# Optimization experiments

Measured on AMD Instinct MI355X. Metric: run time of the kernel, lower is better.

## Reference

```python
import itertools
import jax, jax.numpy as jnp
import numpy as np

GRID = 16384      # self.shape = (GRID,)
LAYERS = 8        # num_layers
SPAN = 2          # span = (2,)
K = 2 * SPAN + 1  # kernel size = 5 (ninputs)
NPOS = 2 ** K     # 32 possible boolean input combos
BATCH = 32
M = 4096          # x width; GRID % M == 0
STRIDE = GRID // M

# bitmask: all 2^K boolean input combinations, shape (NPOS, K)
_BITMASK = jnp.asarray(list(itertools.product(range(2), repeat=K)), dtype=jnp.float32)


def setup_inputs() -> dict:
    key = jax.random.key(0)
    k1, k2 = jax.random.split(key)
    x = jax.random.uniform(k1, (BATCH, M), dtype=jnp.float32)
    toggle_gates = jax.random.uniform(k2, (LAYERS, NPOS, GRID), dtype=jnp.float32)
    return {"x": x, "toggle_gates": toggle_gates}


def _convolve(state):
    # torch convolve(): offsets 0..K-1 via wrap-around roll, then spatial roll by
    # -SPAN to center the window -> neighbor n+i-SPAN (mod GRID) at kernel idx i.
    # jnp.roll(state, SPAN - i) gives out[:, n] = state[:, n + i - SPAN mod GRID].
    return jnp.stack([jnp.roll(state, SPAN - i, axis=1) for i in range(K)], axis=-1)  # (B, N, K)


def reference(x, toggle_gates):
    tw = jax.nn.sigmoid(toggle_gates)  # (L, NPOS, N)
    # embed(): scatter x evenly into the grid, rest is scratch (zeros)
    state = jnp.zeros((x.shape[0], GRID), dtype=x.dtype).at[:, ::STRIDE].set(x)

    def step(s, tw_layer):
        conv = _convolve(s)  # (B, N, K)
        # weight[c, b, n] = prod_i (1 - |bitmask[c, i] - conv[b, n, i]|)
        w = jnp.prod(1.0 - jnp.abs(_BITMASK[:, None, None, :] - conv[None]), axis=-1)  # (C, B, N)
        new = jnp.clip(jnp.einsum('cbn,cn->bn', w, tw_layer), 0.0, 1.0)
        return new, None

    state, _ = jax.lax.scan(step, state, tw)
    # forward returns state[slices] = state[:, ::STRIDE]
    return state[:, ::STRIDE]
```

## Files before the change

kernel.cpp:

```cpp
#include <hip/hip_runtime.h>

#define GRID_N 16384
#define NLAYERS 8
#define NPOS 32
#define BATCH 32
#define MW 4096
#define TILE 32
#define HALO 16
#define WBUF 64
#define ROWP 36

typedef float f2 __attribute__((ext_vector_type(2)));

__device__ __forceinline__ float dpp_shr1(float v) {
    return __builtin_bit_cast(float, __builtin_amdgcn_update_dpp(
        0, __builtin_bit_cast(int, v), 0x138, 0xF, 0xF, true));
}
__device__ __forceinline__ float dpp_shl1(float v) {
    return __builtin_bit_cast(float, __builtin_amdgcn_update_dpp(
        0, __builtin_bit_cast(int, v), 0x130, 0xF, 0xF, true));
}
__device__ __forceinline__ f2 shr1(f2 v) { f2 r; r.x = dpp_shr1(v.x); r.y = dpp_shr1(v.y); return r; }
__device__ __forceinline__ f2 shl1(f2 v) { f2 r; r.x = dpp_shl1(v.x); r.y = dpp_shl1(v.y); return r; }

__device__ __forceinline__ float sigm(float v) {
    return __builtin_amdgcn_rcpf(1.0f + __expf(-v));
}

__device__ __forceinline__ void barrier_lds_only() {
    asm volatile("s_waitcnt lgkmcnt(0)\n\ts_barrier" ::: "memory");
}

__global__ __launch_bounds__(512, 4) void ASIC_44186623541335_kernel(
    const float* __restrict__ x,
    const float* __restrict__ tg,
    float* __restrict__ out)
{
    __shared__ __align__(16) float twl[4][WBUF][ROWP];

    const int tid = threadIdx.x;
    const int tx  = tid & 63;
    const int w   = tid >> 6;
    const int c0  = 4 * w;
    const int start = blockIdx.x * TILE;
    const int gcol  = (start - HALO + tx) & (GRID_N - 1);

    const bool on = (gcol & 3) == 0;
    const int  m  = gcol >> 2;
    float xv[4];
    #pragma unroll
    for (int k = 0; k < 4; ++k)
        xv[k] = on ? x[(c0 + k) * MW + m] : 0.0f;

    float pf[32];
    #pragma unroll
    for (int l = 0; l < NLAYERS; ++l)
        #pragma unroll
        for (int k = 0; k < 4; ++k)
            pf[l * 4 + k] = tg[((size_t)l * NPOS + c0 + k) * GRID_N + gcol];

    f2 S[2];
    S[0].x = xv[0]; S[0].y = xv[1];
    S[1].x = xv[2]; S[1].y = xv[3];

    #pragma unroll
    for (int l4 = 0; l4 < 4; ++l4) {
        float4 sg;
        sg.x = sigm(pf[l4 * 4 + 0]);
        sg.y = sigm(pf[l4 * 4 + 1]);
        sg.z = sigm(pf[l4 * 4 + 2]);
        sg.w = sigm(pf[l4 * 4 + 3]);
        *(float4*)&twl[l4][tx][c0] = sg;
    }
    barrier_lds_only();

    for (int l = 0; l < NLAYERS; ++l) {
        f2 s0v[2], s1v[2], s3v[2], s4v[2];
        #pragma unroll
        for (int q = 0; q < 2; ++q) {
            s1v[q] = shr1(S[q]);
            s0v[q] = shr1(s1v[q]);
            s3v[q] = shl1(S[q]);
            s4v[q] = shl1(s3v[q]);
        }

        f2 u0[16], u1[16];
        #pragma unroll
        for (int k = 0; k < 8; ++k) {
            const float4 t4 = *(const float4*)&twl[l & 3][tx][4 * k];
            const float dA = t4.y - t4.x;
            const float dB = t4.w - t4.z;
            u0[2 * k]     = __builtin_elementwise_fma(s4v[0], (f2)dA, (f2)t4.x);
            u0[2 * k + 1] = __builtin_elementwise_fma(s4v[0], (f2)dB, (f2)t4.z);
            u1[2 * k]     = __builtin_elementwise_fma(s4v[1], (f2)dA, (f2)t4.x);
            u1[2 * k + 1] = __builtin_elementwise_fma(s4v[1], (f2)dB, (f2)t4.z);
        }

        #pragma unroll
        for (int q = 0; q < 2; ++q) {
            f2* u = q ? u1 : u0;
            #pragma unroll
            for (int r = 0; r < 8; ++r)
                u[r] = __builtin_elementwise_fma(s3v[q], u[2 * r + 1] - u[2 * r], u[2 * r]);
            #pragma unroll
            for (int r = 0; r < 4; ++r)
                u[r] = __builtin_elementwise_fma(S[q],   u[2 * r + 1] - u[2 * r], u[2 * r]);
            #pragma unroll
            for (int r = 0; r < 2; ++r)
                u[r] = __builtin_elementwise_fma(s1v[q], u[2 * r + 1] - u[2 * r], u[2 * r]);
            f2 rv = __builtin_elementwise_fma(s0v[q], u[1] - u[0], u[0]);
            rv = __builtin_elementwise_min(__builtin_elementwise_max(rv, (f2)0.0f), (f2)1.0f);
            S[q] = rv;
        }

        if (l == 3) {
            barrier_lds_only();
            #pragma unroll
            for (int l4 = 0; l4 < 4; ++l4) {
                float4 sg;
                sg.x = sigm(pf[16 + l4 * 4 + 0]);
                sg.y = sigm(pf[16 + l4 * 4 + 1]);
                sg.z = sigm(pf[16 + l4 * 4 + 2]);
                sg.w = sigm(pf[16 + l4 * 4 + 3]);
                *(float4*)&twl[l4][tx][c0] = sg;
            }
            barrier_lds_only();
        }
    }

    const int rel = tx - HALO;
    if (rel >= 0 && rel < TILE && (rel & 3) == 0) {
        const int mo = (start >> 2) + (rel >> 2);
        out[(c0 + 0) * MW + mo] = S[0].x;
        out[(c0 + 1) * MW + mo] = S[0].y;
        out[(c0 + 2) * MW + mo] = S[1].x;
        out[(c0 + 3) * MW + mo] = S[1].y;
    }
}

extern "C" void kernel_launch(void* const* d_in, const int* in_sizes, int n_in,
                              void* d_out, int out_size, void* d_ws, size_t ws_size,
                              hipStream_t stream) {
    const float* x  = (const float*)d_in[0];
    const float* tg = (const float*)d_in[1];
    float* out = (float*)d_out;
    ASIC_44186623541335_kernel<<<GRID_N / TILE, 512, 0, stream>>>(x, tg, out);
}
```

Baseline: 80.29 us.

## Stream toggle-gate weights in two-layer groups with rolling register prefetch

```diff
diff --git a/kernel.cpp b/kernel.cpp
--- a/kernel.cpp
+++ b/kernel.cpp
@@ -36,7 +36,7 @@
     const float* __restrict__ tg,
     float* __restrict__ out)
 {
-    __shared__ __align__(16) float twl[4][WBUF][ROWP];
+    __shared__ __align__(16) float twl[2][WBUF][ROWP];
 
     const int tid = threadIdx.x;
     const int tx  = tid & 63;
@@ -52,77 +52,99 @@
     for (int k = 0; k < 4; ++k)
         xv[k] = on ? x[(c0 + k) * MW + m] : 0.0f;
 
-    float pf[32];
+    float pfA[8], pfB[8];
     #pragma unroll
-    for (int l = 0; l < NLAYERS; ++l)
+    for (int ll = 0; ll < 2; ++ll)
         #pragma unroll
         for (int k = 0; k < 4; ++k)
-            pf[l * 4 + k] = tg[((size_t)l * NPOS + c0 + k) * GRID_N + gcol];
+            pfA[ll * 4 + k] = tg[((size_t)ll * NPOS + c0 + k) * GRID_N + gcol];
+    #pragma unroll
+    for (int ll = 0; ll < 2; ++ll)
+        #pragma unroll
+        for (int k = 0; k < 4; ++k)
+            pfB[ll * 4 + k] = tg[((size_t)(2 + ll) * NPOS + c0 + k) * GRID_N + gcol];
 
     f2 S[2];
     S[0].x = xv[0]; S[0].y = xv[1];
     S[1].x = xv[2]; S[1].y = xv[3];
 
     #pragma unroll
-    for (int l4 = 0; l4 < 4; ++l4) {
+    for (int ll = 0; ll < 2; ++ll) {
         float4 sg;
-        sg.x = sigm(pf[l4 * 4 + 0]);
-        sg.y = sigm(pf[l4 * 4 + 1]);
-        sg.z = sigm(pf[l4 * 4 + 2]);
-        sg.w = sigm(pf[l4 * 4 + 3]);
-        *(float4*)&twl[l4][tx][c0] = sg;
+        sg.x = sigm(pfA[ll * 4 + 0]);
+        sg.y = sigm(pfA[ll * 4 + 1]);
+        sg.z = sigm(pfA[ll * 4 + 2]);
+        sg.w = sigm(pfA[ll * 4 + 3]);
+        *(float4*)&twl[ll][tx][c0] = sg;
     }
+    #pragma unroll
+    for (int ll = 0; ll < 2; ++ll)
+        #pragma unroll
+        for (int k = 0; k < 4; ++k)
+            pfA[ll * 4 + k] = tg[((size_t)(4 + ll) * NPOS + c0 + k) * GRID_N + gcol];
     barrier_lds_only();
 
-    for (int l = 0; l < NLAYERS; ++l) {
-        f2 s0v[2], s1v[2], s3v[2], s4v[2];
+    #pragma unroll
+    for (int g = 0; g < 4; ++g) {
         #pragma unroll
-        for (int q = 0; q < 2; ++q) {
-            s1v[q] = shr1(S[q]);
-            s0v[q] = shr1(s1v[q]);
-            s3v[q] = shl1(S[q]);
-            s4v[q] = shl1(s3v[q]);
+        for (int ll = 0; ll < 2; ++ll) {
+            f2 s0v[2], s1v[2], s3v[2], s4v[2];
+            #pragma unroll
+            for (int q = 0; q < 2; ++q) {
+                s1v[q] = shr1(S[q]);
+                s0v[q] = shr1(s1v[q]);
+                s3v[q] = shl1(S[q]);
+                s4v[q] = shl1(s3v[q]);
+            }
+
+            f2 u0[16], u1[16];
+            #pragma unroll
+            for (int k = 0; k < 8; ++k) {
+                const float4 t4 = *(const float4*)&twl[ll][tx][4 * k];
+                const float dA = t4.y - t4.x;
+                const float dB = t4.w - t4.z;
+                u0[2 * k]     = __builtin_elementwise_fma(s4v[0], (f2)dA, (f2)t4.x);
+                u0[2 * k + 1] = __builtin_elementwise_fma(s4v[0], (f2)dB, (f2)t4.z);
+                u1[2 * k]     = __builtin_elementwise_fma(s4v[1], (f2)dA, (f2)t4.x);
+                u1[2 * k + 1] = __builtin_elementwise_fma(s4v[1], (f2)dB, (f2)t4.z);
+            }
+
+            #pragma unroll
+            for (int q = 0; q < 2; ++q) {
+                f2* u = q ? u1 : u0;
+                #pragma unroll
+                for (int r = 0; r < 8; ++r)
+                    u[r] = __builtin_elementwise_fma(s3v[q], u[2 * r + 1] - u[2 * r], u[2 * r]);
+                #pragma unroll
+                for (int r = 0; r < 4; ++r)
+                    u[r] = __builtin_elementwise_fma(S[q],   u[2 * r + 1] - u[2 * r], u[2 * r]);
+                #pragma unroll
+                for (int r = 0; r < 2; ++r)
+                    u[r] = __builtin_elementwise_fma(s1v[q], u[2 * r + 1] - u[2 * r], u[2 * r]);
+                f2 rv = __builtin_elementwise_fma(s0v[q], u[1] - u[0], u[0]);
+                rv = __builtin_elementwise_min(__builtin_elementwise_max(rv, (f2)0.0f), (f2)1.0f);
+                S[q] = rv;
+            }
         }
 
-        f2 u0[16], u1[16];
-        #pragma unroll
-        for (int k = 0; k < 8; ++k) {
-            const float4 t4 = *(const float4*)&twl[l & 3][tx][4 * k];
-            const float dA = t4.y - t4.x;
-            const float dB = t4.w - t4.z;
-            u0[2 * k]     = __builtin_elementwise_fma(s4v[0], (f2)dA, (f2)t4.x);
-            u0[2 * k + 1] = __builtin_elementwise_fma(s4v[0], (f2)dB, (f2)t4.z);
-            u1[2 * k]     = __builtin_elementwise_fma(s4v[1], (f2)dA, (f2)t4.x);
-            u1[2 * k + 1] = __builtin_elementwise_fma(s4v[1], (f2)dB, (f2)t4.z);
-        }
-
-        #pragma unroll
-        for (int q = 0; q < 2; ++q) {
-            f2* u = q ? u1 : u0;
+        if (g < 3) {
+            barrier_lds_only();
+            float* pfs = (g & 1) ? pfA : pfB;
             #pragma unroll
-            for (int r = 0; r < 8; ++r)
-                u[r] = __builtin_elementwise_fma(s3v[q], u[2 * r + 1] - u[2 * r], u[2 * r]);
-            #pragma unroll
-            for (int r = 0; r < 4; ++r)
-                u[r] = __builtin_elementwise_fma(S[q],   u[2 * r + 1] - u[2 * r], u[2 * r]);
-            #pragma unroll
-            for (int r = 0; r < 2; ++r)
-                u[r] = __builtin_elementwise_fma(s1v[q], u[2 * r + 1] - u[2 * r], u[2 * r]);
-            f2 rv = __builtin_elementwise_fma(s0v[q], u[1] - u[0], u[0]);
-            rv = __builtin_elementwise_min(__builtin_elementwise_max(rv, (f2)0.0f), (f2)1.0f);
-            S[q] = rv;
-        }
-
-        if (l == 3) {
-            barrier_lds_only();
-            #pragma unroll
-            for (int l4 = 0; l4 < 4; ++l4) {
+            for (int ll = 0; ll < 2; ++ll) {
                 float4 sg;
-                sg.x = sigm(pf[16 + l4 * 4 + 0]);
-                sg.y = sigm(pf[16 + l4 * 4 + 1]);
-                sg.z = sigm(pf[16 + l4 * 4 + 2]);
-                sg.w = sigm(pf[16 + l4 * 4 + 3]);
-                *(float4*)&twl[l4][tx][c0] = sg;
+                sg.x = sigm(pfs[ll * 4 + 0]);
+                sg.y = sigm(pfs[ll * 4 + 1]);
+                sg.z = sigm(pfs[ll * 4 + 2]);
+                sg.w = sigm(pfs[ll * 4 + 3]);
+                *(float4*)&twl[ll][tx][c0] = sg;
+            }
+            if (g < 1) {
+                #pragma unroll
+                for (int ll = 0; ll < 2; ++ll)
+                    #pragma unroll
+                    for (int k = 0; k < 4; ++k)
+                        pfB[ll * 4 + k] = tg[((size_t)(6 + ll) * NPOS + c0 + k) * GRID_N + gcol];
             }
             barrier_lds_only();
         }
```

Result: no change. 79.70 us (-0.7%).
